# Performance work log

Hardware: AMD Instinct MI355X
Metric: run time of the kernel (lower is better)

## Reference

```python
import jax, jax.numpy as jnp
import numpy as np

EPS = 1e-3  # keras BatchNormalization default epsilon


def _conv1x1(x, W, b):
    # x: (b, h, w, cin), W: (cin, cout)
    return jnp.einsum('bhwc,cd->bhwd', x, W) + b


def _bn(x, gamma, beta, mean, var):
    # inference-mode batch norm (moving statistics)
    return gamma * (x - mean) * jax.lax.rsqrt(var + EPS) + beta


def setup_inputs() -> dict:
    key = jax.random.key(0)
    ks = jax.random.split(key, 20)
    C, Ci = 512, 256
    B, Ha, Wa, Hd, Wd = 8, 32, 32, 64, 64
    s_in = 1.0 / np.sqrt(C)
    s_ic = 1.0 / np.sqrt(Ci)
    inp = {
        'detect': jax.random.normal(ks[0], (B, Hd, Wd, C), jnp.float32),
        'aim': jax.random.normal(ks[1], (B, Ha, Wa, C), jnp.float32),
        # g, theta, phi: C -> Ci 1x1 convs
        'Wg': jax.random.normal(ks[2], (C, Ci), jnp.float32) * s_in,
        'bg': jnp.zeros((Ci,), jnp.float32),
        'Wt': jax.random.normal(ks[3], (C, Ci), jnp.float32) * s_in,
        'bt': jnp.zeros((Ci,), jnp.float32),
        'Wp': jax.random.normal(ks[4], (C, Ci), jnp.float32) * s_in,
        'bp': jnp.zeros((Ci,), jnp.float32),
        # W branch: Ci -> C conv + BN
        'Ww': jax.random.normal(ks[5], (Ci, C), jnp.float32) * s_ic,
        'bw': jnp.zeros((C,), jnp.float32),
        'gw': jnp.ones((C,), jnp.float32),
        'betw': jnp.zeros((C,), jnp.float32),
        'mw': jax.random.normal(ks[6], (C,), jnp.float32) * 0.1,
        'vw': jax.random.uniform(ks[7], (C,), jnp.float32, 0.5, 1.5),
        # Q branch: Ci -> C conv + BN
        'Wq': jax.random.normal(ks[8], (Ci, C), jnp.float32) * s_ic,
        'bq': jnp.zeros((C,), jnp.float32),
        'gq': jnp.ones((C,), jnp.float32),
        'betq': jnp.zeros((C,), jnp.float32),
        'mq': jax.random.normal(ks[9], (C,), jnp.float32) * 0.1,
        'vq': jax.random.uniform(ks[10], (C,), jnp.float32, 0.5, 1.5),
    }
    return inp


def reference(detect, aim, Wg, bg, Wt, bt, Wp, bp,
              Ww, bw, gw, betw, mw, vw,
              Wq, bq, gq, betq, mq, vq):
    B, Ha, Wa, C = aim.shape
    _, Hd, Wd, _ = detect.shape
    Ci = Wg.shape[1]
    Na, Nd = Ha * Wa, Hd * Wd

    d_x = _conv1x1(detect, Wg, bg).reshape(B, Nd, Ci)     # (b, Nd, Ci)
    a_x = _conv1x1(aim, Wg, bg).reshape(B, Na, Ci)        # (b, Na, Ci)
    theta_x = _conv1x1(aim, Wt, bt).reshape(B, Na, Ci)    # (b, Na, Ci)
    phi_x = _conv1x1(detect, Wp, bp).reshape(B, Nd, Ci)   # (b, Nd, Ci)

    # affinity: (b, Na, Nd)
    f = jnp.einsum('bnc,bmc->bnm', theta_x, phi_x)
    f_div_C = f / Nd          # normalize by last dim of f
    fi_div_C = jnp.swapaxes(f, 1, 2) / Na  # (b, Nd, Na), normalized by its last dim

    non_aim = jnp.einsum('bnm,bmc->bnc', f_div_C, d_x).reshape(B, Ha, Wa, Ci)
    non_aim = _bn(_conv1x1(non_aim, Ww, bw), gw, betw, mw, vw) + aim

    non_det = jnp.einsum('bmn,bnc->bmc', fi_div_C, a_x).reshape(B, Hd, Wd, Ci)
    non_det = _bn(_conv1x1(non_det, Wq, bq), gq, betq, mq, vq) + detect

    return non_aim, non_det
```

## Files before the change

kernel.cpp:

```cpp
#include <hip/hip_runtime.h>

typedef unsigned short ushort_t;
typedef unsigned int uint32;
typedef __bf16 bf16x8 __attribute__((ext_vector_type(8)));
typedef float f32x4 __attribute__((ext_vector_type(4)));
typedef uint32 u32x4 __attribute__((ext_vector_type(4)));
typedef uint32 u32x2 __attribute__((ext_vector_type(2)));

typedef __attribute__((address_space(3))) uint32 as3_u32;
typedef const __attribute__((address_space(1))) uint32 as1_u32c;

__device__ __forceinline__ void gl_lds16(const ushort_t* g, ushort_t* l) {
    __builtin_amdgcn_global_load_lds((as1_u32c*)g, (as3_u32*)l, 16, 0, 0);
}

__device__ __forceinline__ float bf2f(ushort_t u) {
    uint32 x = ((uint32)u) << 16;
    return __builtin_bit_cast(float, x);
}
__device__ __forceinline__ ushort_t f2bf(float f) {
    uint32 x = __builtin_bit_cast(uint32, f);
    x += 0x7fffu + ((x >> 16) & 1u);
    return (ushort_t)(x >> 16);
}
__device__ __forceinline__ void ld4bf(const ushort_t* p, float* f) {
    const u32x2 w = *(const u32x2*)p;
    f[0] = bf2f((ushort_t)(w[0] & 0xffffu)); f[1] = bf2f((ushort_t)(w[0] >> 16));
    f[2] = bf2f((ushort_t)(w[1] & 0xffffu)); f[3] = bf2f((ushort_t)(w[1] >> 16));
}
__device__ __forceinline__ u32x2 pk4bf(const float* v) {
    u32x2 pk;
    pk[0] = (uint32)f2bf(v[0]) | ((uint32)f2bf(v[1]) << 16);
    pk[1] = (uint32)f2bf(v[2]) | ((uint32)f2bf(v[3]) << 16);
    return pk;
}

struct VecArgs { const void* s[14]; ushort_t* d[14]; int n[14]; };
__global__ void sniff_vec_kernel(const uint32* __restrict__ src, int* __restrict__ flag,
                                 VecArgs a) {
    __shared__ int cnt;
    if (threadIdx.x == 0) cnt = 0;
    __syncthreads();
    if (threadIdx.x < 64) {
        int weird = 0;
        for (int c = 0; c < 4; c++) {
            uint32 w = src[threadIdx.x * 4 + c];
            uint32 e = (w >> 7) & 0xFFu;
            weird += (e < 64u) || (e >= 192u);
        }
        if (weird) atomicAdd(&cnt, weird);
    }
    __syncthreads();
    const bool isf32 = (cnt > 32);
    if (threadIdx.x == 0) *flag = isf32 ? 1 : 0;
    const int t = threadIdx.x;
    for (int seg = 0; seg < 14; seg++) {
        const int n = a.n[seg];
        if (isf32) {
            const float* s = (const float*)a.s[seg];
            for (int i = t; i < n; i += 256) a.d[seg][i] = f2bf(s[i]);
        } else {
            const ushort_t* s = (const ushort_t*)a.s[seg];
            for (int i = t; i < n; i += 256) a.d[seg][i] = s[i];
        }
    }
}

struct WtArgs { const void* s[6]; ushort_t* d[6]; int R[6]; int C[6]; };
__global__ void canon_all(const void* __restrict__ dsrc, ushort_t* __restrict__ ddst,
                          const void* __restrict__ asrc, ushort_t* __restrict__ adst,
                          WtArgs wa, const int* __restrict__ flag) {
    const bool isf32 = (*flag != 0);
    const int b = blockIdx.x;
    if (b < 3072) {
        const void* src; ushort_t* dst; long n; int b0, nb;
        if (b < 2048) { src = dsrc; dst = ddst; n = 16777216; b0 = b; nb = 2048; }
        else          { src = asrc; dst = adst; n = 4194304;  b0 = b - 2048; nb = 1024; }
        long i = ((long)b0 * 256 + threadIdx.x) * 8;
        const long stride = (long)nb * 256 * 8;
        if (isf32) {
            const float* s = (const float*)src;
            for (; i < n; i += stride) {
                const f32x4 a = *(const f32x4*)(s + i);
                const f32x4 c = *(const f32x4*)(s + i + 4);
                u32x4 o;
                o[0] = (uint32)f2bf(a[0]) | ((uint32)f2bf(a[1]) << 16);
                o[1] = (uint32)f2bf(a[2]) | ((uint32)f2bf(a[3]) << 16);
                o[2] = (uint32)f2bf(c[0]) | ((uint32)f2bf(c[1]) << 16);
                o[3] = (uint32)f2bf(c[2]) | ((uint32)f2bf(c[3]) << 16);
                *(u32x4*)(dst + i) = o;
            }
        } else {
            const ushort_t* s = (const ushort_t*)src;
            for (; i < n; i += stride)
                *(u32x4*)(dst + i) = *(const u32x4*)(s + i);
        }
    } else {
        const int local = b - 3072;
        const int wsel = local >> 8;
        const int rem = local & 255;
        const int tr = rem >> 4, tc = rem & 15;
        const int R = wa.R[wsel], C = wa.C[wsel];
        if (tc * 32 >= C || tr * 32 >= R) return;
        __shared__ float s[32][33];
        const int t = threadIdx.x;
        const int r = t >> 3, c4 = (t & 7) * 4;
        const long sbase = (long)(tr * 32 + r) * C + tc * 32 + c4;
        if (isf32) {
            const float* S = (const float*)wa.s[wsel];
            const f32x4 v = *(const f32x4*)(S + sbase);
            for (int u = 0; u < 4; u++) s[r][c4 + u] = v[u];
        } else {
            const ushort_t* S = (const ushort_t*)wa.s[wsel];
            for (int u = 0; u < 4; u++) s[r][c4 + u] = bf2f(S[sbase + u]);
        }
        __syncthreads();
        float tv[4];
        for (int u = 0; u < 4; u++) tv[u] = s[c4 + u][r];
        *(u32x2*)(wa.d[wsel] + (long)(tc * 32 + r) * R + tr * 32 + c4) = pk4bf(tv);
    }
}

__global__ void reduce_g_kernel(const float* __restrict__ P1, const float* __restrict__ P2,
                                ushort_t* __restrict__ G1, ushort_t* __restrict__ G2) {
    const int bxv = blockIdx.x;
    const int zz = bxv >> 6;
    const float* P = (zz < 8) ? P1 : P2;
    ushort_t* G    = (zz < 8) ? G1 : G2;
    const float alpha = (zz < 8) ? (1.f / 4096.f) : (1.f / 1024.f);
    const int b = zz & 7;
    const long off = ((long)(bxv & 63) * 256 + threadIdx.x) * 4;
    const float* base = P + (long)b * 8 * 65536 + off;
    f32x4 acc = {0.f, 0.f, 0.f, 0.f};
    for (int kc = 0; kc < 8; kc++) acc += *(const f32x4*)(base + (long)kc * 65536);
    float v[4] = {acc[0] * alpha, acc[1] * alpha, acc[2] * alpha, acc[3] * alpha};
    *(u32x2*)(G + (long)b * 65536 + off) = pk4bf(v);
}

#define BM 128
#define BN 128
#define BK 32
#define LDSH (BM * BK)
#define NBUF 3
#define BIGN (1 << 30)

enum { EPI_BIAS = 0, EPI_BIASR = 1, EPI_SCALE = 2, EPI_BN = 3, EPI_PART = 4 };

struct GP {
    const ushort_t* A; const ushort_t* B; void* Cv; ushort_t* CT;
    const ushort_t* bias; const ushort_t* gamma; const ushort_t* beta;
    const ushort_t* mean; const ushort_t* var; const ushort_t* res;
    long coff, sA, sB, sC;
    int K, lda, ldb, ldc, cnmax, ldT, bshift;
    float alpha;
};
struct GP2 { GP g[2]; };

template <int EPI, bool DYNOUT, bool DUALT, bool SWAP>
__global__ __launch_bounds__(256) void gemm_nt(GP2 ga, int ysplit, int zsplit,
                                               const int* __restrict__ flag)
{
    __shared__ __align__(16) ushort_t As[NBUF * LDSH];
    __shared__ __align__(16) ushort_t Bs[NBUF * LDSH];

    const bool isf32 = DYNOUT ? (*flag != 0) : false;

    const uint32 gx = gridDim.x, gy = gridDim.y;
    const uint32 nwg = gx * gy * gridDim.z;
    const uint32 lid = blockIdx.x + gx * (blockIdx.y + gy * blockIdx.z);
    const uint32 swz = (lid & 7u) * (nwg >> 3) + (lid >> 3);
    const uint32 bx = swz % gx, t1 = swz / gx;
    int by = (int)(t1 % gy), bz = (int)(t1 / gy);

    int sel = 0;
    if (by >= ysplit) { by -= ysplit; sel = 1; }
    if (bz >= zsplit) { bz -= zsplit; sel = 1; }
    const GP& p = ga.g[sel];

    const ushort_t* A = p.A + (long)bz * p.sA;
    const ushort_t* B = p.B + ((long)bz + (long)(by >> p.bshift)) * p.sB;
    const long cbase = p.coff + (long)bz * p.sC;
    const int lda = p.lda, ldb = p.ldb, ldc = p.ldc, K = p.K;

    const int tid  = threadIdx.x;
    const int lane = tid & 63;
    const int w    = tid >> 6;
    const int wr   = w >> 1, wc = w & 1;
    const int lr   = lane & 15, q = lane >> 4;

    const int m0 = by * BM;
    const int n0 = bx * BN;

    const int lrow = lane >> 2, lu = lane & 3;
    const int us = (lu ^ ((lrow >> 1) & 3)) * 8;
    const int ra0 = w * 32 + lrow, ra1 = w * 32 + 16 + lrow;
    const ushort_t* Ar0 = A + (long)(m0 + ra0) * lda + us;
    const ushort_t* Ar1 = A + (long)(m0 + ra1) * lda + us;
    const ushort_t* Br0 = B + (long)(n0 + ra0) * ldb + us;
    const ushort_t* Br1 = B + (long)(n0 + ra1) * ldb + us;
    ushort_t* sA0 = &As[(w * 2 + 0) * 512];
    ushort_t* sA1 = &As[(w * 2 + 1) * 512];
    ushort_t* sB0 = &Bs[(w * 2 + 0) * 512];
    ushort_t* sB1 = &Bs[(w * 2 + 1) * 512];

    const int swq = (q ^ ((lr >> 1) & 3)) * 8;

    f32x4 acc[4][4];
#pragma unroll
    for (int i = 0; i < 4; i++)
#pragma unroll
        for (int j = 0; j < 4; j++) acc[i][j] = (f32x4){0.f, 0.f, 0.f, 0.f};

    const int nt = K / BK;
    {
        gl_lds16(Ar0, sA0); gl_lds16(Ar1, sA1);
        gl_lds16(Br0, sB0); gl_lds16(Br1, sB1);
        if (nt > 1) {
            gl_lds16(Ar0 + BK, sA0 + LDSH); gl_lds16(Ar1 + BK, sA1 + LDSH);
            gl_lds16(Br0 + BK, sB0 + LDSH); gl_lds16(Br1 + BK, sB1 + LDSH);
        }
    }

    int c0 = 0, c2 = 2;
    for (int t = 0; t < nt; ++t) {
        if (t + 1 < nt) asm volatile("s_waitcnt vmcnt(4)" ::: "memory");
        else            asm volatile("s_waitcnt vmcnt(0)" ::: "memory");
        __builtin_amdgcn_s_barrier();
        __builtin_amdgcn_sched_barrier(0);

        if (t + 2 < nt) {
            const int nb = c2 * LDSH;
            const int kn = (t + 2) * BK;
            gl_lds16(Ar0 + kn, sA0 + nb); gl_lds16(Ar1 + kn, sA1 + nb);
            gl_lds16(Br0 + kn, sB0 + nb); gl_lds16(Br1 + kn, sB1 + nb);
        }
        __builtin_amdgcn_sched_barrier(0);

        const ushort_t* Ab = As + c0 * LDSH;
        const ushort_t* Bb = Bs + c0 * LDSH;
        bf16x8 af[4], bfr[4];
#pragma unroll
        for (int i = 0; i < 4; i++)
            af[i] = __builtin_bit_cast(bf16x8,
                *(const u32x4*)(&Ab[(wr * 64 + i * 16 + lr) * BK + swq]));
#pragma unroll
        for (int j = 0; j < 4; j++)
            bfr[j] = __builtin_bit_cast(bf16x8,
                *(const u32x4*)(&Bb[(wc * 64 + j * 16 + lr) * BK + swq]));
#pragma unroll
        for (int i = 0; i < 4; i++)
#pragma unroll
            for (int j = 0; j < 4; j++) {
                if constexpr (SWAP)
                    acc[i][j] = __builtin_amdgcn_mfma_f32_16x16x32_bf16(bfr[j], af[i], acc[i][j], 0, 0, 0);
                else
                    acc[i][j] = __builtin_amdgcn_mfma_f32_16x16x32_bf16(af[i], bfr[j], acc[i][j], 0, 0, 0);
            }
        __builtin_amdgcn_sched_barrier(0);

        c0 = (c0 + 1 == NBUF) ? 0 : c0 + 1;
        c2 = (c2 + 1 == NBUF) ? 0 : c2 + 1;
    }

    if constexpr (SWAP) {
#pragma unroll
        for (int j = 0; j < 4; j++) {
            const int coln = n0 + wc * 64 + j * 16 + q * 4;
            float sc4[4], sh4[4];
            if constexpr (EPI == EPI_BIAS) {
                float bb[4]; ld4bf(p.bias + coln, bb);
#pragma unroll
                for (int r = 0; r < 4; r++) { sc4[r] = 1.f; sh4[r] = bb[r]; }
            } else if constexpr (EPI == EPI_SCALE) {
#pragma unroll
                for (int r = 0; r < 4; r++) { sc4[r] = p.alpha; sh4[r] = 0.f; }
            } else if constexpr (EPI == EPI_BN) {
                float bb[4], g[4], bt[4], mn[4], vr[4];
                ld4bf(p.bias + coln, bb); ld4bf(p.gamma + coln, g); ld4bf(p.beta + coln, bt);
                ld4bf(p.mean + coln, mn); ld4bf(p.var + coln, vr);
#pragma unroll
                for (int r = 0; r < 4; r++) {
                    const float s = g[r] * rsqrtf(vr[r] + 1e-3f);
                    sc4[r] = s;
                    sh4[r] = s * bb[r] + bt[r] - s * mn[r];
                }
            }
#pragma unroll
            for (int i = 0; i < 4; i++) {
                const int row = m0 + wr * 64 + i * 16 + lr;
                const long off = cbase + (long)row * ldc + coln;
                float v[4];
#pragma unroll
                for (int r = 0; r < 4; r++) v[r] = acc[i][j][r];
                if constexpr (EPI == EPI_BIASR) {
                    const float bs = bf2f(p.bias[row]);
#pragma unroll
                    for (int r = 0; r < 4; r++) v[r] += bs;
                } else if constexpr (EPI == EPI_BN) {
                    float rs[4]; ld4bf(p.res + (long)row * ldc + coln, rs);
#pragma unroll
                    for (int r = 0; r < 4; r++) v[r] = sc4[r] * v[r] + sh4[r] + rs[r];
                } else if constexpr (EPI != EPI_PART) {
#pragma unroll
                    for (int r = 0; r < 4; r++) v[r] = sc4[r] * v[r] + sh4[r];
                }
                if constexpr (EPI == EPI_PART) {
                    *(f32x4*)((float*)p.Cv + off) = (f32x4){v[0], v[1], v[2], v[3]};
                } else if constexpr (DYNOUT) {
                    if (isf32) *(f32x4*)((float*)p.Cv + off) = (f32x4){v[0], v[1], v[2], v[3]};
                    else       *(u32x2*)((ushort_t*)p.Cv + off) = pk4bf(v);
                } else {
                    *(u32x2*)((ushort_t*)p.Cv + off) = pk4bf(v);
                }
            }
        }
    } else {
        const bool doC = (n0 < p.cnmax);
#pragma unroll
        for (int j = 0; j < 4; j++) {
            const int col = n0 + wc * 64 + j * 16 + lr;
            float bs = 0.f;
            if constexpr (EPI == EPI_BIAS) bs = bf2f(p.bias[col]);
#pragma unroll
            for (int i = 0; i < 4; i++) {
                const int rowbase = m0 + wr * 64 + i * 16 + q * 4;
                ushort_t tmp[4];
#pragma unroll
                for (int r = 0; r < 4; r++) {
                    const int row = rowbase + r;
                    float v = acc[i][j][r];
                    if constexpr (EPI == EPI_BIAS) v += bs;
                    else if constexpr (EPI == EPI_BIASR) v += bf2f(p.bias[row]);
                    else if constexpr (EPI == EPI_SCALE) v *= p.alpha;
                    const long off = cbase + (long)row * ldc + col;
                    if constexpr (EPI == EPI_PART) {
                        ((float*)p.Cv)[off] = v;
                    } else {
                        const ushort_t us2 = f2bf(v);
                        tmp[r] = us2;
                        if (doC) ((ushort_t*)p.Cv)[off] = us2;
                    }
                }
                if constexpr (DUALT) {
                    u32x2 pk;
                    pk[0] = (uint32)tmp[0] | ((uint32)tmp[1] << 16);
                    pk[1] = (uint32)tmp[2] | ((uint32)tmp[3] << 16);
                    *(u32x2*)(p.CT + (long)bz * p.sC + (long)col * p.ldT + rowbase) = pk;
                }
            }
        }
    }
}

extern "C" void kernel_launch(void* const* d_in, const int* in_sizes, int n_in,
                              void* d_out, int out_size, void* d_ws, size_t ws_size,
                              hipStream_t stream)
{
    int* flag = (int*)d_ws;
    ushort_t* base = (ushort_t*)((char*)d_ws + 16);
    long o = 0;
    ushort_t* detect_c = base + o; o += 16777216;
    ushort_t* aim_c    = base + o; o += 4194304;
    ushort_t* WpgT = base + o; o += 262144;
    ushort_t* WtgT = base + o; o += 262144;
    ushort_t* WwT  = base + o; o += 131072;
    ushort_t* WqT  = base + o; o += 131072;
    ushort_t* bpg_c  = base + o; o += 512;
    ushort_t* btg_c  = base + o; o += 512;
    ushort_t* bw_c   = base + o; o += 512;
    ushort_t* gw_c   = base + o; o += 512;
    ushort_t* betw_c = base + o; o += 512;
    ushort_t* mw_c   = base + o; o += 512;
    ushort_t* vw_c   = base + o; o += 512;
    ushort_t* bq_c   = base + o; o += 512;
    ushort_t* gq_c   = base + o; o += 512;
    ushort_t* betq_c = base + o; o += 512;
    ushort_t* mq_c   = base + o; o += 512;
    ushort_t* vq_c   = base + o; o += 512;
    ushort_t* phi    = base + o; o += 8388608;
    ushort_t* PT     = base + o; o += 16777216;
    ushort_t* theta  = base + o; o += 2097152;
    ushort_t* TT     = base + o; o += 4194304;
    ushort_t* G1     = base + o; o += 524288;
    ushort_t* G2     = base + o; o += 524288;
    ushort_t* M1T    = base + o; o += 1048576;
    ushort_t* M2T    = base + o; o += 1048576;
    ushort_t* U      = base + o; o += 16777216;
    float* P1 = (float*)U;
    float* P2 = P1 + 4194304;
    ushort_t* phiT = PT;
    ushort_t* d_xT = PT + 8388608;
    ushort_t* thetaT = TT;
    ushort_t* a_xT = TT + 2097152;

    VecArgs va;
    const int vidx[14] = {7, 3, 5, 3, 9, 10, 11, 12, 13, 15, 16, 17, 18, 19};
    ushort_t* vdst[14] = {bpg_c, bpg_c + 256, btg_c, btg_c + 256,
                          bw_c, gw_c, betw_c, mw_c, vw_c,
                          bq_c, gq_c, betq_c, mq_c, vq_c};
    const int vn[14] = {256, 256, 256, 256, 512, 512, 512, 512, 512, 512, 512, 512, 512, 512};
    for (int i = 0; i < 14; i++) { va.s[i] = d_in[vidx[i]]; va.d[i] = vdst[i]; va.n[i] = vn[i]; }
    sniff_vec_kernel<<<1, 256, 0, stream>>>((const uint32*)d_in[0], flag, va);

    WtArgs wa;
    wa.s[0] = d_in[6];  wa.d[0] = WpgT;              wa.R[0] = 512; wa.C[0] = 256;
    wa.s[1] = d_in[2];  wa.d[1] = WpgT + 256 * 512;  wa.R[1] = 512; wa.C[1] = 256;
    wa.s[2] = d_in[4];  wa.d[2] = WtgT;              wa.R[2] = 512; wa.C[2] = 256;
    wa.s[3] = d_in[2];  wa.d[3] = WtgT + 256 * 512;  wa.R[3] = 512; wa.C[3] = 256;
    wa.s[4] = d_in[8];  wa.d[4] = WwT;               wa.R[4] = 256; wa.C[4] = 512;
    wa.s[5] = d_in[14]; wa.d[5] = WqT;               wa.R[5] = 256; wa.C[5] = 512;
    canon_all<<<4608, 256, 0, stream>>>(d_in[0], detect_c, d_in[1], aim_c, wa, flag);

    const dim3 blk(256);
    const ushort_t* np = nullptr;
    ushort_t* npm = nullptr;

    {
        GP2 g;
        g.g[0] = GP{detect_c, WpgT, phi, PT, bpg_c, np, np, np, np, np,
                    0, 0, 0, 0, 512, 512, 512, 256, 256, 32768, 30, 1.f};
        g.g[1] = GP{aim_c, WtgT, theta, TT, btg_c, np, np, np, np, np,
                    0, 0, 0, 0, 512, 512, 512, 256, 256, 8192, 30, 1.f};
        gemm_nt<EPI_BIAS, false, true, false><<<dim3(4, 320, 1), blk, 0, stream>>>(
            g, 256, BIGN, flag);
    }

    {
        GP2 g;
        g.g[0] = GP{phiT, d_xT, P1, npm, np, np, np, np, np, np,
                    0, 512, 512, 65536, 512, 32768, 32768, 256, BIGN, 0, 30, 1.f};
        g.g[1] = GP{thetaT, a_xT, P2, npm, np, np, np, np, np, np,
                    0, 128, 128, 65536, 128, 8192, 8192, 256, BIGN, 0, 30, 1.f};
        gemm_nt<EPI_PART, false, false, true><<<dim3(2, 2, 128), blk, 0, stream>>>(
            g, BIGN, 64, flag);
    }

    reduce_g_kernel<<<1024, blk, 0, stream>>>(P1, P2, G1, G2);

    {
        GP2 g;
        g.g[0] = GP{G1, WwT, npm, M1T, np, np, np, np, np, np,
                    0, 65536, 0, 131072, 256, 256, 256, 512, 0, 256, 30, 1.f};
        g.g[1] = GP{G2, WqT, npm, M2T, np, np, np, np, np, np,
                    0, 65536, 0, 131072, 256, 256, 256, 512, 0, 256, 30, 1.f};
        gemm_nt<EPI_SCALE, false, true, false><<<dim3(4, 2, 16), blk, 0, stream>>>(
            g, BIGN, 8, flag);
    }

    {
        GP2 g;
        g.g[0] = GP{phi, M2T, d_out, npm, bq_c, gq_c, betq_c, mq_c, vq_c, detect_c,
                    8192L * 512, 0, 131072, 0, 256, 256, 256, 512, BIGN, 0, 5, 1.f};
        g.g[1] = GP{theta, M1T, d_out, npm, bw_c, gw_c, betw_c, mw_c, vw_c, aim_c,
                    0, 0, 131072, 0, 256, 256, 256, 512, BIGN, 0, 3, 1.f};
        gemm_nt<EPI_BN, true, false, true><<<dim3(4, 320, 1), blk, 0, stream>>>(
            g, 256, BIGN, flag);
    }
}
```

Baseline: 352.4 us.

## Fuse fp32-to-bf16 input conversion into projection GEMM A-loads and residual epilogue

Drops the separate pass that converted detect/aim into bf16 workspace copies. The first projection GEMM now reads the fp32 activations directly through registers, converts them and writes LDS with a two-buffer syncthreads pipeline. The final BN epilogue reads the fp32 residual directly. This removes a full read/write of the large activations, but the A-side load in that GEMM loses the async global-to-LDS three-stage pipeline and reads twice as many bytes per tile.

Result: slower. 369.6 us (+4.9%).

```diff
diff --git a/kernel.cpp b/kernel.cpp
--- a/kernel.cpp
+++ b/kernel.cpp
@@ -67,58 +67,28 @@
 }
 
 struct WtArgs { const void* s[6]; ushort_t* d[6]; int R[6]; int C[6]; };
-__global__ void canon_all(const void* __restrict__ dsrc, ushort_t* __restrict__ ddst,
-                          const void* __restrict__ asrc, ushort_t* __restrict__ adst,
-                          WtArgs wa, const int* __restrict__ flag) {
+__global__ void wt_canon_all(WtArgs a, const int* __restrict__ flag) {
+    const int wsel = blockIdx.z;
+    const int R = a.R[wsel], C = a.C[wsel];
+    const int tr = blockIdx.y, tc = blockIdx.x;
+    if (tc * 32 >= C || tr * 32 >= R) return;
+    __shared__ float s[32][33];
     const bool isf32 = (*flag != 0);
-    const int b = blockIdx.x;
-    if (b < 3072) {
-        const void* src; ushort_t* dst; long n; int b0, nb;
-        if (b < 2048) { src = dsrc; dst = ddst; n = 16777216; b0 = b; nb = 2048; }
-        else          { src = asrc; dst = adst; n = 4194304;  b0 = b - 2048; nb = 1024; }
-        long i = ((long)b0 * 256 + threadIdx.x) * 8;
-        const long stride = (long)nb * 256 * 8;
-        if (isf32) {
-            const float* s = (const float*)src;
-            for (; i < n; i += stride) {
-                const f32x4 a = *(const f32x4*)(s + i);
-                const f32x4 c = *(const f32x4*)(s + i + 4);
-                u32x4 o;
-                o[0] = (uint32)f2bf(a[0]) | ((uint32)f2bf(a[1]) << 16);
-                o[1] = (uint32)f2bf(a[2]) | ((uint32)f2bf(a[3]) << 16);
-                o[2] = (uint32)f2bf(c[0]) | ((uint32)f2bf(c[1]) << 16);
-                o[3] = (uint32)f2bf(c[2]) | ((uint32)f2bf(c[3]) << 16);
-                *(u32x4*)(dst + i) = o;
-            }
-        } else {
-            const ushort_t* s = (const ushort_t*)src;
-            for (; i < n; i += stride)
-                *(u32x4*)(dst + i) = *(const u32x4*)(s + i);
-        }
+    const int t = threadIdx.x;
+    const int r = t >> 3, c4 = (t & 7) * 4;
+    const long sbase = (long)(tr * 32 + r) * C + tc * 32 + c4;
+    if (isf32) {
+        const float* S = (const float*)a.s[wsel];
+        const f32x4 v = *(const f32x4*)(S + sbase);
+        for (int u = 0; u < 4; u++) s[r][c4 + u] = v[u];
     } else {
-        const int local = b - 3072;
-        const int wsel = local >> 8;
-        const int rem = local & 255;
-        const int tr = rem >> 4, tc = rem & 15;
-        const int R = wa.R[wsel], C = wa.C[wsel];
-        if (tc * 32 >= C || tr * 32 >= R) return;
-        __shared__ float s[32][33];
-        const int t = threadIdx.x;
-        const int r = t >> 3, c4 = (t & 7) * 4;
-        const long sbase = (long)(tr * 32 + r) * C + tc * 32 + c4;
-        if (isf32) {
-            const float* S = (const float*)wa.s[wsel];
-            const f32x4 v = *(const f32x4*)(S + sbase);
-            for (int u = 0; u < 4; u++) s[r][c4 + u] = v[u];
-        } else {
-            const ushort_t* S = (const ushort_t*)wa.s[wsel];
-            for (int u = 0; u < 4; u++) s[r][c4 + u] = bf2f(S[sbase + u]);
-        }
-        __syncthreads();
-        float tv[4];
-        for (int u = 0; u < 4; u++) tv[u] = s[c4 + u][r];
-        *(u32x2*)(wa.d[wsel] + (long)(tc * 32 + r) * R + tr * 32 + c4) = pk4bf(tv);
-    }
+        const ushort_t* S = (const ushort_t*)a.s[wsel];
+        for (int u = 0; u < 4; u++) s[r][c4 + u] = bf2f(S[sbase + u]);
+    }
+    __syncthreads();
+    float tv[4];
+    for (int u = 0; u < 4; u++) tv[u] = s[c4 + u][r];
+    *(u32x2*)(a.d[wsel] + (long)(tc * 32 + r) * R + tr * 32 + c4) = pk4bf(tv);
 }
 
 __global__ void reduce_g_kernel(const float* __restrict__ P1, const float* __restrict__ P2,
@@ -156,14 +126,14 @@
 };
 struct GP2 { GP g[2]; };
 
-template <int EPI, bool DYNOUT, bool DUALT, bool SWAP>
+template <int EPI, bool DYNOUT, bool DUALT, bool SWAP, bool AF32>
 __global__ __launch_bounds__(256) void gemm_nt(GP2 ga, int ysplit, int zsplit,
                                                const int* __restrict__ flag)
 {
     __shared__ __align__(16) ushort_t As[NBUF * LDSH];
     __shared__ __align__(16) ushort_t Bs[NBUF * LDSH];
 
-    const bool isf32 = DYNOUT ? (*flag != 0) : false;
+    const bool isf32 = (DYNOUT || AF32) ? (*flag != 0) : false;
 
     const uint32 gx = gridDim.x, gy = gridDim.y;
     const uint32 nwg = gx * gy * gridDim.z;
@@ -178,6 +148,7 @@
     const GP& p = ga.g[sel];
 
     const ushort_t* A = p.A + (long)bz * p.sA;
+    const float* A32 = (const float*)p.A + (long)bz * p.sA;
     const ushort_t* B = p.B + ((long)bz + (long)(by >> p.bshift)) * p.sB;
     const long cbase = p.coff + (long)bz * p.sC;
     const int lda = p.lda, ldb = p.ldb, ldc = p.ldc, K = p.K;
@@ -194,8 +165,8 @@
     const int lrow = lane >> 2, lu = lane & 3;
     const int us = (lu ^ ((lrow >> 1) & 3)) * 8;
     const int ra0 = w * 32 + lrow, ra1 = w * 32 + 16 + lrow;
-    const ushort_t* Ar0 = A + (long)(m0 + ra0) * lda + us;
-    const ushort_t* Ar1 = A + (long)(m0 + ra1) * lda + us;
+    const long ao0 = (long)(m0 + ra0) * lda + us;
+    const long ao1 = (long)(m0 + ra1) * lda + us;
     const ushort_t* Br0 = B + (long)(n0 + ra0) * ldb + us;
     const ushort_t* Br1 = B + (long)(n0 + ra1) * ldb + us;
     ushort_t* sA0 = &As[(w * 2 + 0) * 512];
@@ -212,54 +183,124 @@
         for (int j = 0; j < 4; j++) acc[i][j] = (f32x4){0.f, 0.f, 0.f, 0.f};
 
     const int nt = K / BK;
-    {
-        gl_lds16(Ar0, sA0); gl_lds16(Ar1, sA1);
+
+    if constexpr (AF32) {
+        f32x4 raw[4];
+        u32x4 rb0, rb1;
+        auto loadA = [&](int kk) {
+            if (isf32) {
+                const float* s0 = A32 + ao0 + kk;
+                const float* s1 = A32 + ao1 + kk;
+                raw[0] = *(const f32x4*)s0; raw[1] = *(const f32x4*)(s0 + 4);
+                raw[2] = *(const f32x4*)s1; raw[3] = *(const f32x4*)(s1 + 4);
+            } else {
+                rb0 = *(const u32x4*)(A + ao0 + kk);
+                rb1 = *(const u32x4*)(A + ao1 + kk);
+            }
+        };
+        auto writeA = [&](int buf) {
+            ushort_t* d0 = sA0 + buf * LDSH + lane * 8;
+            ushort_t* d1 = sA0 + buf * LDSH + 512 + lane * 8;
+            if (isf32) {
+                u32x4 o0, o1;
+                o0[0] = (uint32)f2bf(raw[0][0]) | ((uint32)f2bf(raw[0][1]) << 16);
+                o0[1] = (uint32)f2bf(raw[0][2]) | ((uint32)f2bf(raw[0][3]) << 16);
+                o0[2] = (uint32)f2bf(raw[1][0]) | ((uint32)f2bf(raw[1][1]) << 16);
+                o0[3] = (uint32)f2bf(raw[1][2]) | ((uint32)f2bf(raw[1][3]) << 16);
+                o1[0] = (uint32)f2bf(raw[2][0]) | ((uint32)f2bf(raw[2][1]) << 16);
+                o1[1] = (uint32)f2bf(raw[2][2]) | ((uint32)f2bf(raw[2][3]) << 16);
+                o1[2] = (uint32)f2bf(raw[3][0]) | ((uint32)f2bf(raw[3][1]) << 16);
+                o1[3] = (uint32)f2bf(raw[3][2]) | ((uint32)f2bf(raw[3][3]) << 16);
+                *(u32x4*)d0 = o0; *(u32x4*)d1 = o1;
+            } else {
+                *(u32x4*)d0 = rb0; *(u32x4*)d1 = rb1;
+            }
+        };
+        loadA(0);
         gl_lds16(Br0, sB0); gl_lds16(Br1, sB1);
-        if (nt > 1) {
-            gl_lds16(Ar0 + BK, sA0 + LDSH); gl_lds16(Ar1 + BK, sA1 + LDSH);
-            gl_lds16(Br0 + BK, sB0 + LDSH); gl_lds16(Br1 + BK, sB1 + LDSH);
-        }
-    }
-
-    int c0 = 0, c2 = 2;
-    for (int t = 0; t < nt; ++t) {
-        if (t + 1 < nt) asm volatile("s_waitcnt vmcnt(4)" ::: "memory");
-        else            asm volatile("s_waitcnt vmcnt(0)" ::: "memory");
-        __builtin_amdgcn_s_barrier();
-        __builtin_amdgcn_sched_barrier(0);
-
-        if (t + 2 < nt) {
-            const int nb = c2 * LDSH;
-            const int kn = (t + 2) * BK;
-            gl_lds16(Ar0 + kn, sA0 + nb); gl_lds16(Ar1 + kn, sA1 + nb);
-            gl_lds16(Br0 + kn, sB0 + nb); gl_lds16(Br1 + kn, sB1 + nb);
-        }
-        __builtin_amdgcn_sched_barrier(0);
-
-        const ushort_t* Ab = As + c0 * LDSH;
-        const ushort_t* Bb = Bs + c0 * LDSH;
-        bf16x8 af[4], bfr[4];
-#pragma unroll
-        for (int i = 0; i < 4; i++)
-            af[i] = __builtin_bit_cast(bf16x8,
-                *(const u32x4*)(&Ab[(wr * 64 + i * 16 + lr) * BK + swq]));
-#pragma unroll
-        for (int j = 0; j < 4; j++)
-            bfr[j] = __builtin_bit_cast(bf16x8,
-                *(const u32x4*)(&Bb[(wc * 64 + j * 16 + lr) * BK + swq]));
-#pragma unroll
-        for (int i = 0; i < 4; i++)
-#pragma unroll
-            for (int j = 0; j < 4; j++) {
-                if constexpr (SWAP)
-                    acc[i][j] = __builtin_amdgcn_mfma_f32_16x16x32_bf16(bfr[j], af[i], acc[i][j], 0, 0, 0);
-                else
-                    acc[i][j] = __builtin_amdgcn_mfma_f32_16x16x32_bf16(af[i], bfr[j], acc[i][j], 0, 0, 0);
-            }
-        __builtin_amdgcn_sched_barrier(0);
-
-        c0 = (c0 + 1 == NBUF) ? 0 : c0 + 1;
-        c2 = (c2 + 1 == NBUF) ? 0 : c2 + 1;
+        for (int t = 0; t < nt; ++t) {
+            const int cur = t & 1;
+            writeA(cur);
+            __syncthreads();
+            if (t + 1 < nt) {
+                loadA((t + 1) * BK);
+                const int nb = (cur ^ 1) * LDSH;
+                gl_lds16(Br0 + (t + 1) * BK, sB0 + nb);
+                gl_lds16(Br1 + (t + 1) * BK, sB1 + nb);
+            }
+            const ushort_t* Ab = As + cur * LDSH;
+            const ushort_t* Bb = Bs + cur * LDSH;
+            bf16x8 af[4], bfr[4];
+#pragma unroll
+            for (int i = 0; i < 4; i++)
+                af[i] = __builtin_bit_cast(bf16x8,
+                    *(const u32x4*)(&Ab[(wr * 64 + i * 16 + lr) * BK + swq]));
+#pragma unroll
+            for (int j = 0; j < 4; j++)
+                bfr[j] = __builtin_bit_cast(bf16x8,
+                    *(const u32x4*)(&Bb[(wc * 64 + j * 16 + lr) * BK + swq]));
+#pragma unroll
+            for (int i = 0; i < 4; i++)
+#pragma unroll
+                for (int j = 0; j < 4; j++) {
+                    if constexpr (SWAP)
+                        acc[i][j] = __builtin_amdgcn_mfma_f32_16x16x32_bf16(bfr[j], af[i], acc[i][j], 0, 0, 0);
+                    else
+                        acc[i][j] = __builtin_amdgcn_mfma_f32_16x16x32_bf16(af[i], bfr[j], acc[i][j], 0, 0, 0);
+                }
+            __syncthreads();
+        }
+    } else {
+        const ushort_t* Ar0 = A + ao0;
+        const ushort_t* Ar1 = A + ao1;
+        {
+            gl_lds16(Ar0, sA0); gl_lds16(Ar1, sA1);
+            gl_lds16(Br0, sB0); gl_lds16(Br1, sB1);
+            if (nt > 1) {
+                gl_lds16(Ar0 + BK, sA0 + LDSH); gl_lds16(Ar1 + BK, sA1 + LDSH);
+                gl_lds16(Br0 + BK, sB0 + LDSH); gl_lds16(Br1 + BK, sB1 + LDSH);
+            }
+        }
+        int c0 = 0, c2 = 2;
+        for (int t = 0; t < nt; ++t) {
+            if (t + 1 < nt) asm volatile("s_waitcnt vmcnt(4)" ::: "memory");
+            else            asm volatile("s_waitcnt vmcnt(0)" ::: "memory");
+            __builtin_amdgcn_s_barrier();
+            __builtin_amdgcn_sched_barrier(0);
+
+            if (t + 2 < nt) {
+                const int nb = c2 * LDSH;
+                const int kn = (t + 2) * BK;
+                gl_lds16(Ar0 + kn, sA0 + nb); gl_lds16(Ar1 + kn, sA1 + nb);
+                gl_lds16(Br0 + kn, sB0 + nb); gl_lds16(Br1 + kn, sB1 + nb);
+            }
+            __builtin_amdgcn_sched_barrier(0);
+
+            const ushort_t* Ab = As + c0 * LDSH;
+            const ushort_t* Bb = Bs + c0 * LDSH;
+            bf16x8 af[4], bfr[4];
+#pragma unroll
+            for (int i = 0; i < 4; i++)
+                af[i] = __builtin_bit_cast(bf16x8,
+                    *(const u32x4*)(&Ab[(wr * 64 + i * 16 + lr) * BK + swq]));
+#pragma unroll
+            for (int j = 0; j < 4; j++)
+                bfr[j] = __builtin_bit_cast(bf16x8,
+                    *(const u32x4*)(&Bb[(wc * 64 + j * 16 + lr) * BK + swq]));
+#pragma unroll
+            for (int i = 0; i < 4; i++)
+#pragma unroll
+                for (int j = 0; j < 4; j++) {
+                    if constexpr (SWAP)
+                        acc[i][j] = __builtin_amdgcn_mfma_f32_16x16x32_bf16(bfr[j], af[i], acc[i][j], 0, 0, 0);
+                    else
+                        acc[i][j] = __builtin_amdgcn_mfma_f32_16x16x32_bf16(af[i], bfr[j], acc[i][j], 0, 0, 0);
+                }
+            __builtin_amdgcn_sched_barrier(0);
+
+            c0 = (c0 + 1 == NBUF) ? 0 : c0 + 1;
+            c2 = (c2 + 1 == NBUF) ? 0 : c2 + 1;
+        }
     }
 
     if constexpr (SWAP) {
@@ -297,7 +338,14 @@
 #pragma unroll
                     for (int r = 0; r < 4; r++) v[r] += bs;
                 } else if constexpr (EPI == EPI_BN) {
-                    float rs[4]; ld4bf(p.res + (long)row * ldc + coln, rs);
+                    float rs[4];
+                    if (isf32) {
+                        const f32x4 rv = *(const f32x4*)((const float*)p.res + (long)row * ldc + coln);
+#pragma unroll
+                        for (int r = 0; r < 4; r++) rs[r] = rv[r];
+                    } else {
+                        ld4bf(p.res + (long)row * ldc + coln, rs);
+                    }
 #pragma unroll
                     for (int r = 0; r < 4; r++) v[r] = sc4[r] * v[r] + sh4[r] + rs[r];
                 } else if constexpr (EPI != EPI_PART) {
@@ -359,8 +407,6 @@
     int* flag = (int*)d_ws;
     ushort_t* base = (ushort_t*)((char*)d_ws + 16);
     long o = 0;
-    ushort_t* detect_c = base + o; o += 16777216;
-    ushort_t* aim_c    = base + o; o += 4194304;
     ushort_t* WpgT = base + o; o += 262144;
     ushort_t* WtgT = base + o; o += 262144;
     ushort_t* WwT  = base + o; o += 131072;
@@ -409,7 +455,7 @@
     wa.s[3] = d_in[2];  wa.d[3] = WtgT + 256 * 512;  wa.R[3] = 512; wa.C[3] = 256;
     wa.s[4] = d_in[8];  wa.d[4] = WwT;               wa.R[4] = 256; wa.C[4] = 512;
     wa.s[5] = d_in[14]; wa.d[5] = WqT;               wa.R[5] = 256; wa.C[5] = 512;
-    canon_all<<<4608, 256, 0, stream>>>(d_in[0], detect_c, d_in[1], aim_c, wa, flag);
+    wt_canon_all<<<dim3(16, 16, 6), 256, 0, stream>>>(wa, flag);
 
     const dim3 blk(256);
     const ushort_t* np = nullptr;
@@ -417,11 +463,11 @@
 
     {
         GP2 g;
-        g.g[0] = GP{detect_c, WpgT, phi, PT, bpg_c, np, np, np, np, np,
+        g.g[0] = GP{(const ushort_t*)d_in[0], WpgT, phi, PT, bpg_c, np, np, np, np, np,
                     0, 0, 0, 0, 512, 512, 512, 256, 256, 32768, 30, 1.f};
-        g.g[1] = GP{aim_c, WtgT, theta, TT, btg_c, np, np, np, np, np,
+        g.g[1] = GP{(const ushort_t*)d_in[1], WtgT, theta, TT, btg_c, np, np, np, np, np,
                     0, 0, 0, 0, 512, 512, 512, 256, 256, 8192, 30, 1.f};
-        gemm_nt<EPI_BIAS, false, true, false><<<dim3(4, 320, 1), blk, 0, stream>>>(
+        gemm_nt<EPI_BIAS, false, true, false, true><<<dim3(4, 320, 1), blk, 0, stream>>>(
             g, 256, BIGN, flag);
     }
 
@@ -431,7 +477,7 @@
                     0, 512, 512, 65536, 512, 32768, 32768, 256, BIGN, 0, 30, 1.f};
         g.g[1] = GP{thetaT, a_xT, P2, npm, np, np, np, np, np, np,
                     0, 128, 128, 65536, 128, 8192, 8192, 256, BIGN, 0, 30, 1.f};
-        gemm_nt<EPI_PART, false, false, true><<<dim3(2, 2, 128), blk, 0, stream>>>(
+        gemm_nt<EPI_PART, false, false, true, false><<<dim3(2, 2, 128), blk, 0, stream>>>(
             g, BIGN, 64, flag);
     }
 
@@ -443,17 +489,19 @@
                     0, 65536, 0, 131072, 256, 256, 256, 512, 0, 256, 30, 1.f};
         g.g[1] = GP{G2, WqT, npm, M2T, np, np, np, np, np, np,
                     0, 65536, 0, 131072, 256, 256, 256, 512, 0, 256, 30, 1.f};
-        gemm_nt<EPI_SCALE, false, true, false><<<dim3(4, 2, 16), blk, 0, stream>>>(
+        gemm_nt<EPI_SCALE, false, true, false, false><<<dim3(4, 2, 16), blk, 0, stream>>>(
             g, BIGN, 8, flag);
     }
 
     {
         GP2 g;
-        g.g[0] = GP{phi, M2T, d_out, npm, bq_c, gq_c, betq_c, mq_c, vq_c, detect_c,
+        g.g[0] = GP{phi, M2T, d_out, npm, bq_c, gq_c, betq_c, mq_c, vq_c,
+                    (const ushort_t*)d_in[0],
                     8192L * 512, 0, 131072, 0, 256, 256, 256, 512, BIGN, 0, 5, 1.f};
-        g.g[1] = GP{theta, M1T, d_out, npm, bw_c, gw_c, betw_c, mw_c, vw_c, aim_c,
+        g.g[1] = GP{theta, M1T, d_out, npm, bw_c, gw_c, betw_c, mw_c, vw_c,
+                    (const ushort_t*)d_in[1],
                     0, 0, 131072, 0, 256, 256, 256, 512, BIGN, 0, 3, 1.f};
-        gemm_nt<EPI_BN, true, false, true><<<dim3(4, 320, 1), blk, 0, stream>>>(
+        gemm_nt<EPI_BN, true, false, true, false><<<dim3(4, 320, 1), blk, 0, stream>>>(
             g, 256, BIGN, flag);
     }
 }
```
